# Performance work log

Measured on AMD Instinct MI355X. Metric: run time of the kernel, lower is better.

The kernel has to match this reference:

```python
import jax, jax.numpy as jnp
import numpy as np

QB = 127.0  # 8-bit symmetric activation range (input_bits=8)
EPS = 1e-5


def _weight_quant_ternary(w):
    # weight_quant_new: s = 1/mean(|w|); round(w*s).clamp(-1,1)
    s = 1.0 / jnp.clip(jnp.mean(jnp.abs(w)), EPS, None)
    return jnp.clip(jnp.round(w * s), -1.0, 1.0)


def setup_inputs() -> dict:
    key = jax.random.key(0)
    kx, kw = jax.random.split(key)
    B, S, IN, OUT = 4, 2048, 4096, 4096
    x = jax.random.normal(kx, (B, S, IN), dtype=jnp.float32)
    w_raw = jax.random.normal(kw, (OUT, IN), dtype=jnp.float32)
    # Module stores pre-quantized (packed) ternary weights as a buffer.
    w = _weight_quant_ternary(w_raw)  # values in {-1, 0, 1}, shape [OUT, IN]
    scale = jnp.float32(1.0)
    return {"x": x, "w": w, "scale": scale}


def reference(x, w, scale):
    # BitNet-style forward: per-token absmax int8 activation quantization,
    # ternary-weight matmul, then dequantize and apply module scale.
    gamma = jnp.clip(jnp.max(jnp.abs(x), axis=-1, keepdims=True), EPS, None)  # [B,S,1]
    x_q = jnp.clip(jnp.round(x * (QB / gamma)), -QB, QB)  # int8-valued floats
    y = jnp.einsum('bsi,oi->bso', x_q, w)  # low-bit GEMM accumulate
    return y * (gamma / QB) * scale
```

## Files before the change

kernel.cpp:

```cpp
#include <hip/hip_runtime.h>
#include <hip/hip_bf16.h>
#include <stdint.h>

#define QB 127.0f
#define EPS_G 1e-5f
#define K_DIM 4096
#define N_DIM 4096
#define BM 128
#define BN 128
#define BK 64

typedef int v4i __attribute__((ext_vector_type(4)));

#define GLOAD16(gp, lp)                                                        \
  __builtin_amdgcn_global_load_lds(                                            \
      (const __attribute__((address_space(1))) void*)(gp),                     \
      (__attribute__((address_space(3))) void*)(lp), 16, 0, 0)

__global__ __launch_bounds__(256) void quant_w_kernel(
    const float* __restrict__ w, signed char* __restrict__ wq) {
  const int idx = blockIdx.x * 256 + threadIdx.x;
  const float4 v = ((const float4*)w)[idx];
  char4 q;
  q.x = (signed char)(int)v.x;
  q.y = (signed char)(int)v.y;
  q.z = (signed char)(int)v.z;
  q.w = (signed char)(int)v.w;
  ((char4*)wq)[idx] = q;
}

__global__ __launch_bounds__(256) void quant_x_kernel(
    const float* __restrict__ x, signed char* __restrict__ xq,
    float* __restrict__ gamma_out) {
  const int row = blockIdx.x;
  const int t = threadIdx.x;
  const float4* xr = (const float4*)(x + (size_t)row * K_DIM);
  float4 v[4];
  float m = 0.f;
#pragma unroll
  for (int i = 0; i < 4; ++i) {
    v[i] = xr[t + i * 256];
    m = fmaxf(m, fmaxf(fmaxf(fabsf(v[i].x), fabsf(v[i].y)),
                       fmaxf(fabsf(v[i].z), fabsf(v[i].w))));
  }
#pragma unroll
  for (int o = 32; o > 0; o >>= 1) m = fmaxf(m, __shfl_xor(m, o));
  __shared__ float red[4];
  if ((t & 63) == 0) red[t >> 6] = m;
  __syncthreads();
  m = fmaxf(fmaxf(red[0], red[1]), fmaxf(red[2], red[3]));
  const float gamma = fmaxf(m, EPS_G);
  if (t == 0) gamma_out[row] = gamma;
  const float inv = QB / gamma;
  char4* xqr = (char4*)(xq + (size_t)row * K_DIM);
#pragma unroll
  for (int i = 0; i < 4; ++i) {
    const float a = fminf(fmaxf(rintf(v[i].x * inv), -QB), QB);
    const float b = fminf(fmaxf(rintf(v[i].y * inv), -QB), QB);
    const float c = fminf(fmaxf(rintf(v[i].z * inv), -QB), QB);
    const float d = fminf(fmaxf(rintf(v[i].w * inv), -QB), QB);
    char4 q;
    q.x = (signed char)(int)a;
    q.y = (signed char)(int)b;
    q.z = (signed char)(int)c;
    q.w = (signed char)(int)d;
    xqr[t + i * 256] = q;
  }
}

__global__ __launch_bounds__(256) void gemm_i8_kernel(
    const signed char* __restrict__ A,
    const signed char* __restrict__ Bq,
    const float* __restrict__ gamma,
    const float* __restrict__ scale_p,
    float* __restrict__ C,
    int M) {
  __shared__ signed char lA[BM * BK];
  __shared__ signed char lB[BN * BK];

  const int t = threadIdx.x;
  const int lane = t & 63;
  const int wave = t >> 6;
  const int wr = wave >> 1;
  const int wc = wave & 1;

  const int nwg = gridDim.x;
  const int q8 = nwg >> 3;
  const int bid = blockIdx.x;
  const int swz = (bid & 7) * q8 + (bid >> 3);
  const int nbx = N_DIM / BN;
  const int brow = (swz / nbx) * BM;
  const int bcol = (swz % nbx) * BN;

  const int c0 = t, c1 = t + 256;
  const signed char* gA0 = A + (size_t)(brow + (c0 >> 2)) * K_DIM + (c0 & 3) * 16;
  const signed char* gA1 = A + (size_t)(brow + (c1 >> 2)) * K_DIM + (c1 & 3) * 16;
  const signed char* gB0 = Bq + (size_t)(bcol + (c0 >> 2)) * K_DIM + (c0 & 3) * 16;
  const signed char* gB1 = Bq + (size_t)(bcol + (c1 >> 2)) * K_DIM + (c1 & 3) * 16;

  signed char* lAp0 = &lA[wave * 1024];
  signed char* lAp1 = &lA[4096 + wave * 1024];
  signed char* lBp0 = &lB[wave * 1024];
  signed char* lBp1 = &lB[4096 + wave * 1024];

  v4i acc[4][4];
#pragma unroll
  for (int i = 0; i < 4; ++i)
#pragma unroll
    for (int j = 0; j < 4; ++j) acc[i][j] = (v4i){0, 0, 0, 0};

  const int ar = wr * 64 + (lane & 15);
  const int br = wc * 64 + (lane & 15);
  const int ks = (lane >> 4) * 16;

  for (int k0 = 0; k0 < K_DIM; k0 += BK) {
    GLOAD16(gA0 + k0, lAp0);
    GLOAD16(gA1 + k0, lAp1);
    GLOAD16(gB0 + k0, lBp0);
    GLOAD16(gB1 + k0, lBp1);
    __syncthreads();

    v4i af[4], bf[4];
#pragma unroll
    for (int m = 0; m < 4; ++m)
      af[m] = *(const v4i*)&lA[(ar + m * 16) * BK + ks];
#pragma unroll
    for (int n = 0; n < 4; ++n)
      bf[n] = *(const v4i*)&lB[(br + n * 16) * BK + ks];

#pragma unroll
    for (int m = 0; m < 4; ++m)
#pragma unroll
      for (int n = 0; n < 4; ++n)
        acc[m][n] =
            __builtin_amdgcn_mfma_i32_16x16x64_i8(af[m], bf[n], acc[m][n], 0, 0, 0);
    __syncthreads();
  }

  const float scl = *scale_p;
  const int col0 = bcol + wc * 64 + (lane & 15);
  const int row0 = brow + wr * 64 + ((lane >> 4) << 2);
#pragma unroll
  for (int m = 0; m < 4; ++m) {
#pragma unroll
    for (int j = 0; j < 4; ++j) {
      const int row = row0 + m * 16 + j;
      const float g = gamma[row] / QB;
#pragma unroll
      for (int n = 0; n < 4; ++n) {
        const int col = col0 + n * 16;
        C[(size_t)row * N_DIM + col] = ((float)acc[m][n][j] * g) * scl;
      }
    }
  }
}

extern "C" void kernel_launch(void* const* d_in, const int* in_sizes, int n_in,
                              void* d_out, int out_size, void* d_ws, size_t ws_size,
                              hipStream_t stream) {
  const float* x = (const float*)d_in[0];
  const float* w = (const float*)d_in[1];
  const float* scale = (const float*)d_in[2];
  float* out = (float*)d_out;

  const int M = in_sizes[0] / K_DIM;

  signed char* wq = (signed char*)d_ws;
  signed char* xq = wq + (size_t)N_DIM * K_DIM;
  float* gamma = (float*)(xq + (size_t)M * K_DIM);

  quant_w_kernel<<<(N_DIM * K_DIM / 4) / 256, 256, 0, stream>>>(w, wq);
  quant_x_kernel<<<M, 256, 0, stream>>>(x, xq, gamma);

  const int nwg = (M / BM) * (N_DIM / BN);
  gemm_i8_kernel<<<nwg, 256, 0, stream>>>(xq, wq, gamma, scale, out, M);
}
```

Measured before the change: 418.0 us.

## Rewrite int8 GEMM as 256x256 eight-phase pipelined kernel and fuse quant kernels

Replaces the simple 128x128 int8 MFMA GEMM with a 256x256-tile, 512-thread kernel. It uses 128 KB of double-buffered, XOR-swizzled LDS, an eight-phase schedule that interleaves global-to-LDS loads with MFMA work, explicit waitcnt, barriers and setprio, and nontemporal output stores. The weight and activation quantization kernels are merged into one launch. The aim is more data reuse per tile, no LDS bank conflicts, and memory latency hidden behind compute, at the cost of fragile hand scheduling, heavy register pressure, and a swizzle that hardcodes the grid to 512 blocks.

Measured after the change: 383.4 us. 1.09x faster.

```diff
diff --git a/kernel.cpp b/kernel.cpp
--- a/kernel.cpp
+++ b/kernel.cpp
@@ -4,11 +4,13 @@
 
 #define QB 127.0f
 #define EPS_G 1e-5f
-#define K_DIM 4096
-#define N_DIM 4096
-#define BM 128
-#define BN 128
-#define BK 64
+#define KD 4096
+#define ND 4096
+#define BM 256
+#define BN 256
+#define BKB 128
+#define NT (KD / BKB)
+#define NI (NT / 2)
 
 typedef int v4i __attribute__((ext_vector_type(4)));
 
@@ -17,142 +19,199 @@
       (const __attribute__((address_space(1))) void*)(gp),                     \
       (__attribute__((address_space(3))) void*)(lp), 16, 0, 0)
 
-__global__ __launch_bounds__(256) void quant_w_kernel(
-    const float* __restrict__ w, signed char* __restrict__ wq) {
-  const int idx = blockIdx.x * 256 + threadIdx.x;
-  const float4 v = ((const float4*)w)[idx];
-  char4 q;
-  q.x = (signed char)(int)v.x;
-  q.y = (signed char)(int)v.y;
-  q.z = (signed char)(int)v.z;
-  q.w = (signed char)(int)v.w;
-  ((char4*)wq)[idx] = q;
-}
-
-__global__ __launch_bounds__(256) void quant_x_kernel(
-    const float* __restrict__ x, signed char* __restrict__ xq,
-    float* __restrict__ gamma_out) {
-  const int row = blockIdx.x;
+#define BAR  __builtin_amdgcn_s_barrier()
+#define SB0  __builtin_amdgcn_sched_barrier(0)
+#define WLG0 asm volatile("s_waitcnt lgkmcnt(0)" ::: "memory")
+#define WLG8 asm volatile("s_waitcnt lgkmcnt(8)" ::: "memory")
+#define WVM4 asm volatile("s_waitcnt vmcnt(4)" ::: "memory")
+
+__global__ __launch_bounds__(256) void quant_fused_kernel(
+    const float* __restrict__ x, const float* __restrict__ w,
+    signed char* __restrict__ xq, signed char* __restrict__ wq,
+    float* __restrict__ gamma_out, int M) {
+  const int b = blockIdx.x;
   const int t = threadIdx.x;
-  const float4* xr = (const float4*)(x + (size_t)row * K_DIM);
-  float4 v[4];
-  float m = 0.f;
-#pragma unroll
-  for (int i = 0; i < 4; ++i) {
-    v[i] = xr[t + i * 256];
-    m = fmaxf(m, fmaxf(fmaxf(fabsf(v[i].x), fabsf(v[i].y)),
-                       fmaxf(fabsf(v[i].z), fabsf(v[i].w))));
-  }
-#pragma unroll
-  for (int o = 32; o > 0; o >>= 1) m = fmaxf(m, __shfl_xor(m, o));
-  __shared__ float red[4];
-  if ((t & 63) == 0) red[t >> 6] = m;
-  __syncthreads();
-  m = fmaxf(fmaxf(red[0], red[1]), fmaxf(red[2], red[3]));
-  const float gamma = fmaxf(m, EPS_G);
-  if (t == 0) gamma_out[row] = gamma;
-  const float inv = QB / gamma;
-  char4* xqr = (char4*)(xq + (size_t)row * K_DIM);
-#pragma unroll
-  for (int i = 0; i < 4; ++i) {
-    const float a = fminf(fmaxf(rintf(v[i].x * inv), -QB), QB);
-    const float b = fminf(fmaxf(rintf(v[i].y * inv), -QB), QB);
-    const float c = fminf(fmaxf(rintf(v[i].z * inv), -QB), QB);
-    const float d = fminf(fmaxf(rintf(v[i].w * inv), -QB), QB);
-    char4 q;
-    q.x = (signed char)(int)a;
-    q.y = (signed char)(int)b;
-    q.z = (signed char)(int)c;
-    q.w = (signed char)(int)d;
-    xqr[t + i * 256] = q;
+  if (b < M) {
+    const float4* xr = (const float4*)(x + (size_t)b * KD);
+    float4 v[4];
+    float m = 0.f;
+#pragma unroll
+    for (int i = 0; i < 4; ++i) {
+      v[i] = xr[t + i * 256];
+      m = fmaxf(m, fmaxf(fmaxf(fabsf(v[i].x), fabsf(v[i].y)),
+                         fmaxf(fabsf(v[i].z), fabsf(v[i].w))));
+    }
+#pragma unroll
+    for (int o = 32; o > 0; o >>= 1) m = fmaxf(m, __shfl_xor(m, o));
+    __shared__ float red[4];
+    if ((t & 63) == 0) red[t >> 6] = m;
+    __syncthreads();
+    m = fmaxf(fmaxf(red[0], red[1]), fmaxf(red[2], red[3]));
+    const float gamma = fmaxf(m, EPS_G);
+    if (t == 0) gamma_out[b] = gamma;
+    const float inv = QB / gamma;
+    char4* xqr = (char4*)(xq + (size_t)b * KD);
+#pragma unroll
+    for (int i = 0; i < 4; ++i) {
+      char4 q;
+      q.x = (signed char)(int)fminf(fmaxf(rintf(v[i].x * inv), -QB), QB);
+      q.y = (signed char)(int)fminf(fmaxf(rintf(v[i].y * inv), -QB), QB);
+      q.z = (signed char)(int)fminf(fmaxf(rintf(v[i].z * inv), -QB), QB);
+      q.w = (signed char)(int)fminf(fmaxf(rintf(v[i].w * inv), -QB), QB);
+      xqr[t + i * 256] = q;
+    }
+  } else {
+    const int row = b - M;
+    const float4* wr_ = (const float4*)(w + (size_t)row * KD);
+    char4* wqr = (char4*)(wq + (size_t)row * KD);
+#pragma unroll
+    for (int i = 0; i < 4; ++i) {
+      const float4 v = wr_[t + i * 256];
+      char4 q;
+      q.x = (signed char)(int)v.x;
+      q.y = (signed char)(int)v.y;
+      q.z = (signed char)(int)v.z;
+      q.w = (signed char)(int)v.w;
+      wqr[t + i * 256] = q;
+    }
   }
 }
 
-__global__ __launch_bounds__(256) void gemm_i8_kernel(
+__global__ __launch_bounds__(512, 2) void gemm_i8_8ph_kernel(
     const signed char* __restrict__ A,
-    const signed char* __restrict__ Bq,
+    const signed char* __restrict__ B,
     const float* __restrict__ gamma,
     const float* __restrict__ scale_p,
-    float* __restrict__ C,
-    int M) {
-  __shared__ signed char lA[BM * BK];
-  __shared__ signed char lB[BN * BK];
+    float* __restrict__ C) {
+  extern __shared__ signed char lds[];
+  signed char* ldsA = lds;
+  signed char* ldsB = lds + 65536;
 
   const int t = threadIdx.x;
   const int lane = t & 63;
   const int wave = t >> 6;
-  const int wr = wave >> 1;
-  const int wc = wave & 1;
-
-  const int nwg = gridDim.x;
-  const int q8 = nwg >> 3;
+  const int wr = wave >> 2;
+  const int wcol = wave & 3;
+  const int lr = lane & 15;
+  const int lc = (lane >> 4) << 4;
+  const int swzm = (lr & 7) << 4;
+
   const int bid = blockIdx.x;
-  const int swz = (bid & 7) * q8 + (bid >> 3);
-  const int nbx = N_DIM / BN;
-  const int brow = (swz / nbx) * BM;
-  const int bcol = (swz % nbx) * BN;
-
-  const int c0 = t, c1 = t + 256;
-  const signed char* gA0 = A + (size_t)(brow + (c0 >> 2)) * K_DIM + (c0 & 3) * 16;
-  const signed char* gA1 = A + (size_t)(brow + (c1 >> 2)) * K_DIM + (c1 & 3) * 16;
-  const signed char* gB0 = Bq + (size_t)(bcol + (c0 >> 2)) * K_DIM + (c0 & 3) * 16;
-  const signed char* gB1 = Bq + (size_t)(bcol + (c1 >> 2)) * K_DIM + (c1 & 3) * 16;
-
-  signed char* lAp0 = &lA[wave * 1024];
-  signed char* lAp1 = &lA[4096 + wave * 1024];
-  signed char* lBp0 = &lB[wave * 1024];
-  signed char* lBp1 = &lB[4096 + wave * 1024];
-
-  v4i acc[4][4];
-#pragma unroll
-  for (int i = 0; i < 4; ++i)
+  const int swz = (bid & 7) * 64 + (bid >> 3);
+  const int brow = (swz >> 4) * BM;
+  const int bcol = (swz & 15) * BN;
+
+  const int c0 = t, c1 = t + 512;
+  const int r0 = c0 >> 3, r1 = c1 >> 3;
+  const int g0 = ((c0 & 7) << 4) ^ ((r0 & 7) << 4);
+  const int g1 = ((c1 & 7) << 4) ^ ((r1 & 7) << 4);
+  const signed char* sA0 = A + (size_t)(brow + r0) * KD + g0;
+  const signed char* sA1 = A + (size_t)(brow + r1) * KD + g1;
+  const signed char* sB0 = B + (size_t)(bcol + r0) * KD + g0;
+  const signed char* sB1 = B + (size_t)(bcol + r1) * KD + g1;
+
+#define STAGE_A(d, h, kt)                                                      \
+  do {                                                                         \
+    GLOAD16(sA0 + (size_t)(h) * 128 * KD + (kt) * BKB,                         \
+            ldsA + (d) * 32768 + (h) * 16384 + c0 * 16);                       \
+    GLOAD16(sA1 + (size_t)(h) * 128 * KD + (kt) * BKB,                         \
+            ldsA + (d) * 32768 + (h) * 16384 + c1 * 16);                       \
+  } while (0)
+#define STAGE_B(d, h, kt)                                                      \
+  do {                                                                         \
+    GLOAD16(sB0 + (size_t)(h) * 128 * KD + (kt) * BKB,                         \
+            ldsB + (d) * 32768 + (h) * 16384 + c0 * 16);                       \
+    GLOAD16(sB1 + (size_t)(h) * 128 * KD + (kt) * BKB,                         \
+            ldsB + (d) * 32768 + (h) * 16384 + c1 * 16);                       \
+  } while (0)
+
+#define LDA_H(d, mh)                                                           \
+  _Pragma("unroll") for (int m_ = 0; m_ < 4; ++m_)                             \
+  _Pragma("unroll") for (int k_ = 0; k_ < 2; ++k_)                             \
+    af[m_][k_] = *(const v4i*)(ldsA + (d) * 32768 +                            \
+        (wr * 128 + (mh) * 64 + m_ * 16 + lr) * 128 + ((k_ * 64 + lc) ^ swzm))
+#define LDB_P(d, nh)                                                           \
+  _Pragma("unroll") for (int n_ = 0; n_ < 2; ++n_)                             \
+  _Pragma("unroll") for (int k_ = 0; k_ < 2; ++k_)                             \
+    bf[(nh) * 2 + n_][k_] = *(const v4i*)(ldsB + (d) * 32768 +                 \
+        (wcol * 64 + (nh) * 32 + n_ * 16 + lr) * 128 + ((k_ * 64 + lc) ^ swzm))
+
+#define MFMA_Q(mh, nh)                                                         \
+  do {                                                                         \
+    __builtin_amdgcn_s_setprio(1);                                             \
+    _Pragma("unroll") for (int m_ = 0; m_ < 4; ++m_)                           \
+    _Pragma("unroll") for (int n_ = 0; n_ < 2; ++n_)                           \
+    _Pragma("unroll") for (int k_ = 0; k_ < 2; ++k_)                           \
+      acc[(mh) * 4 + m_][(nh) * 2 + n_] = __builtin_amdgcn_mfma_i32_16x16x64_i8( \
+          af[m_][k_], bf[(nh) * 2 + n_][k_], acc[(mh) * 4 + m_][(nh) * 2 + n_], \
+          0, 0, 0);                                                            \
+    __builtin_amdgcn_s_setprio(0);                                             \
+  } while (0)
+
+  v4i acc[8][4];
+#pragma unroll
+  for (int i = 0; i < 8; ++i)
 #pragma unroll
     for (int j = 0; j < 4; ++j) acc[i][j] = (v4i){0, 0, 0, 0};
-
-  const int ar = wr * 64 + (lane & 15);
-  const int br = wc * 64 + (lane & 15);
-  const int ks = (lane >> 4) * 16;
-
-  for (int k0 = 0; k0 < K_DIM; k0 += BK) {
-    GLOAD16(gA0 + k0, lAp0);
-    GLOAD16(gA1 + k0, lAp1);
-    GLOAD16(gB0 + k0, lBp0);
-    GLOAD16(gB1 + k0, lBp1);
-    __syncthreads();
-
-    v4i af[4], bf[4];
-#pragma unroll
-    for (int m = 0; m < 4; ++m)
-      af[m] = *(const v4i*)&lA[(ar + m * 16) * BK + ks];
-#pragma unroll
-    for (int n = 0; n < 4; ++n)
-      bf[n] = *(const v4i*)&lB[(br + n * 16) * BK + ks];
-
-#pragma unroll
-    for (int m = 0; m < 4; ++m)
-#pragma unroll
-      for (int n = 0; n < 4; ++n)
-        acc[m][n] =
-            __builtin_amdgcn_mfma_i32_16x16x64_i8(af[m], bf[n], acc[m][n], 0, 0, 0);
-    __syncthreads();
+  v4i af[4][2], bf[4][2];
+
+  STAGE_B(0, 0, 0); STAGE_B(0, 1, 0); STAGE_A(0, 0, 0); STAGE_A(0, 1, 0);
+  STAGE_B(1, 0, 1); STAGE_B(1, 1, 1);
+  WVM4;
+  BAR; SB0;
+
+#pragma unroll 1
+  for (int i = 0; i < NI; ++i) {
+    const int kc1 = 2 * i + 1;
+    const int kn2 = (2 * i + 2) & (NT - 1);
+    const int kn3 = (2 * i + 3) & (NT - 1);
+
+    LDA_H(0, 0); LDB_P(0, 0); STAGE_A(1, 0, kc1); WLG8;
+    BAR; WLG0; SB0; MFMA_Q(0, 0); SB0; BAR; SB0;
+
+    LDB_P(0, 1); STAGE_A(1, 1, kc1);
+    BAR; WLG0; SB0; MFMA_Q(0, 1); SB0; BAR; SB0;
+
+    LDA_H(0, 1); STAGE_B(0, 0, kn2);
+    BAR; WLG0; SB0; MFMA_Q(1, 0); SB0; BAR; SB0;
+
+    STAGE_B(0, 1, kn2); WVM4;
+    BAR; SB0; MFMA_Q(1, 1); SB0; BAR; SB0;
+
+    LDA_H(1, 0); LDB_P(1, 0); STAGE_A(0, 0, kn2); WLG8;
+    BAR; WLG0; SB0; MFMA_Q(0, 0); SB0; BAR; SB0;
+
+    LDB_P(1, 1); STAGE_A(0, 1, kn2);
+    BAR; WLG0; SB0; MFMA_Q(0, 1); SB0; BAR; SB0;
+
+    LDA_H(1, 1); STAGE_B(1, 0, kn3);
+    BAR; WLG0; SB0; MFMA_Q(1, 0); SB0; BAR; SB0;
+
+    STAGE_B(1, 1, kn3); WVM4;
+    BAR; SB0; MFMA_Q(1, 1); SB0; BAR; SB0;
   }
 
   const float scl = *scale_p;
-  const int col0 = bcol + wc * 64 + (lane & 15);
-  const int row0 = brow + wr * 64 + ((lane >> 4) << 2);
-#pragma unroll
-  for (int m = 0; m < 4; ++m) {
+  const int ccol0 = bcol + wcol * 64 + lr;
+  const int crow0 = brow + wr * 128 + (lane >> 4) * 4;
+#pragma unroll
+  for (int m_ = 0; m_ < 8; ++m_) {
 #pragma unroll
     for (int j = 0; j < 4; ++j) {
-      const int row = row0 + m * 16 + j;
+      const int row = crow0 + m_ * 16 + j;
       const float g = gamma[row] / QB;
 #pragma unroll
-      for (int n = 0; n < 4; ++n) {
-        const int col = col0 + n * 16;
-        C[(size_t)row * N_DIM + col] = ((float)acc[m][n][j] * g) * scl;
+      for (int n_ = 0; n_ < 4; ++n_) {
+        __builtin_nontemporal_store(((float)acc[m_][n_][j] * g) * scl,
+                                    &C[(size_t)row * ND + ccol0 + n_ * 16]);
       }
     }
   }
+#undef STAGE_A
+#undef STAGE_B
+#undef LDA_H
+#undef LDB_P
+#undef MFMA_Q
 }
 
 extern "C" void kernel_launch(void* const* d_in, const int* in_sizes, int n_in,
@@ -163,15 +222,14 @@
   const float* scale = (const float*)d_in[2];
   float* out = (float*)d_out;
 
-  const int M = in_sizes[0] / K_DIM;
+  const int M = in_sizes[0] / KD;
 
   signed char* wq = (signed char*)d_ws;
-  signed char* xq = wq + (size_t)N_DIM * K_DIM;
-  float* gamma = (float*)(xq + (size_t)M * K_DIM);
-
-  quant_w_kernel<<<(N_DIM * K_DIM / 4) / 256, 256, 0, stream>>>(w, wq);
-  quant_x_kernel<<<M, 256, 0, stream>>>(x, xq, gamma);
-
-  const int nwg = (M / BM) * (N_DIM / BN);
-  gemm_i8_kernel<<<nwg, 256, 0, stream>>>(xq, wq, gamma, scale, out, M);
+  signed char* xq = wq + (size_t)ND * KD;
+  float* gamma = (float*)(xq + (size_t)M * KD);
+
+  quant_fused_kernel<<<M + ND, 256, 0, stream>>>(x, w, xq, wq, gamma, M);
+
+  const int nwg = (M / BM) * (ND / BN);
+  gemm_i8_8ph_kernel<<<nwg, 512, 131072, stream>>>(xq, wq, gamma, scale, out);
 }
```
